# Kernel optimization log

Measured on AMD Instinct MI355X. Metric: run time of the kernel, lower is better.

Reference implementation:

```python
import jax, jax.numpy as jnp
import numpy as np

V, D, H, L, T, B = 32000, 512, 8, 4, 2048, 2
HS = D // H


def setup_inputs() -> dict:
    key = jax.random.key(0)
    ks = jax.random.split(key, 10)
    s = 0.02  # init std, per _init_weights
    rn = lambda k, shape: jax.random.normal(k, shape, jnp.float32) * s
    return {
        "idx": jax.random.randint(ks[0], (B, T), 0, V),
        "tok_emb": rn(ks[1], (V, D)),
        "pos_emb": rn(ks[2], (T, D)),
        "ln1_g": jnp.ones((L, D)), "ln1_b": jnp.zeros((L, D)),
        "wq": rn(ks[3], (L, D, D)), "wk": rn(ks[4], (L, D, D)), "wv": rn(ks[5], (L, D, D)),
        "wo": rn(ks[6], (L, D, D)), "bo": jnp.zeros((L, D)),
        "ln2_g": jnp.ones((L, D)), "ln2_b": jnp.zeros((L, D)),
        "w1": rn(ks[7], (L, D, 4 * D)), "b1": jnp.zeros((L, 4 * D)),
        "w2": rn(ks[8], (L, 4 * D, D)), "b2": jnp.zeros((L, D)),
        "lnf_g": jnp.ones((D,)), "lnf_b": jnp.zeros((D,)),
        "head_w": rn(ks[9], (D, V)), "head_b": jnp.zeros((V,)),
    }


def _ln(x, g, b):
    mu = x.mean(-1, keepdims=True)
    var = ((x - mu) ** 2).mean(-1, keepdims=True)
    return (x - mu) * jax.lax.rsqrt(var + 1e-5) * g + b


def reference(idx, tok_emb, pos_emb, ln1_g, ln1_b, wq, wk, wv, wo, bo,
              ln2_g, ln2_b, w1, b1, w2, b2, lnf_g, lnf_b, head_w, head_b):
    Bb, Tt = idx.shape
    x = tok_emb[idx] + pos_emb[jnp.arange(Tt)]  # [B,T,D]
    mask = jnp.tril(jnp.ones((Tt, Tt), bool))
    scale = HS ** -0.5

    def block(x, p):
        g1, bb1, Wq, Wk, Wv, Wo, Bo, g2, bb2, W1, B1, W2, B2 = p
        h = _ln(x, g1, bb1)
        q = (h @ Wq).reshape(Bb, Tt, H, HS)
        k = (h @ Wk).reshape(Bb, Tt, H, HS)
        v = (h @ Wv).reshape(Bb, Tt, H, HS)
        wei = jnp.einsum('bthd,bshd->bhts', q, k) * scale  # [B,H,T,T]
        wei = jnp.where(mask, wei, -jnp.inf)
        wei = jax.nn.softmax(wei, axis=-1)
        att = jnp.einsum('bhts,bshd->bthd', wei, v).reshape(Bb, Tt, D)
        x = x + att @ Wo + Bo
        h2 = _ln(x, g2, bb2)
        x = x + jax.nn.relu(h2 @ W1 + B1) @ W2 + B2
        return x, None

    x, _ = jax.lax.scan(block, x, (ln1_g, ln1_b, wq, wk, wv, wo, bo,
                                   ln2_g, ln2_b, w1, b1, w2, b2))
    logits = _ln(x, lnf_g, lnf_b) @ head_w + head_b  # [B,T,V]
    return logits
```

## Files before the change

### kernel.cpp

```cpp
#include <hip/hip_runtime.h>
#include <hip/hip_bf16.h>
#include <cstddef>

typedef __bf16 bf16;
typedef __attribute__((ext_vector_type(8))) __bf16 bf16x8;
typedef __attribute__((ext_vector_type(4))) __bf16 bf16x4;
typedef __attribute__((ext_vector_type(4))) float f32x4;

constexpr int VOC = 32000;
constexpr int DIM = 512;
constexpr int NH  = 8;
constexpr int HSZ = 64;
constexpr int SEQ = 2048;
constexpr int NB  = 2;
constexpr int NL  = 4;
constexpr int NTOK = NB * SEQ;
constexpr int QS  = 3 * DIM;
constexpr int QKS = 2 * DIM;

__device__ __forceinline__ void gload16(const void* g, void* lds) {
  __builtin_amdgcn_global_load_lds(
      (const __attribute__((address_space(1))) unsigned int*)g,
      (__attribute__((address_space(3))) unsigned int*)lds, 16, 0, 0);
}

__global__ __launch_bounds__(256) void wt_emln(
    const int* __restrict__ idx, const float* __restrict__ tok,
    const float* __restrict__ pos, const float* __restrict__ g1,
    const float* __restrict__ b1v, float* __restrict__ x, bf16* __restrict__ h,
    const float* __restrict__ wq, const float* __restrict__ wk,
    const float* __restrict__ wv, const float* __restrict__ wo,
    const float* __restrict__ w1, const float* __restrict__ w2,
    const float* __restrict__ hw,
    bf16* __restrict__ wqkvT, bf16* __restrict__ woT,
    bf16* __restrict__ w1T, bf16* __restrict__ w2T, bf16* __restrict__ headT) {
  __shared__ float t[32][33];
  __shared__ float s1[4], s2[4];
  int bid = blockIdx.x;
  int tid = threadIdx.x;
  if (bid < NTOK) {
    int row = bid;
    int lane = tid & 63, w = tid >> 6;
    int tt = row & (SEQ - 1);
    int tk = idx[row];
    float a0 = tok[(size_t)tk * DIM + tid] + pos[(size_t)tt * DIM + tid];
    float a1 = tok[(size_t)tk * DIM + tid + 256] + pos[(size_t)tt * DIM + tid + 256];
    x[(size_t)row * DIM + tid] = a0;
    x[(size_t)row * DIM + tid + 256] = a1;
    float ps = a0 + a1, pq = a0 * a0 + a1 * a1;
#pragma unroll
    for (int m = 1; m < 64; m <<= 1) {
      ps += __shfl_xor(ps, m, 64);
      pq += __shfl_xor(pq, m, 64);
    }
    if (lane == 0) { s1[w] = ps; s2[w] = pq; }
    __syncthreads();
    float fs = s1[0] + s1[1] + s1[2] + s1[3];
    float fq = s2[0] + s2[1] + s2[2] + s2[3];
    float mu = fs * (1.0f / DIM);
    float var = fq * (1.0f / DIM) - mu * mu;
    float rs = rsqrtf(var + 1e-5f);
    h[(size_t)row * DIM + tid] = (bf16)((a0 - mu) * rs * g1[tid] + b1v[tid]);
    h[(size_t)row * DIM + tid + 256] =
        (bf16)((a1 - mu) * rs * g1[tid + 256] + b1v[tid + 256]);
    return;
  }
  int wb = bid - NTOK;
  const float* src; bf16* dst; int K, N, n0, k0;
  if (wb < 12288) {
    int l = wb / 3072, tt = wb - l * 3072;
    if (tt < 1024) {
      int which = tt >> 8, u = tt & 255;
      K = DIM; N = DIM;
      n0 = (u & 15) * 32; k0 = (u >> 4) * 32;
      if (which == 0)      { src = wq + (size_t)l * DIM * DIM; dst = wqkvT + (size_t)l * QS * DIM; }
      else if (which == 1) { src = wk + (size_t)l * DIM * DIM; dst = wqkvT + (size_t)l * QS * DIM + DIM * DIM; }
      else if (which == 2) { src = wv + (size_t)l * DIM * DIM; dst = wqkvT + (size_t)l * QS * DIM + 2 * DIM * DIM; }
      else                 { src = wo + (size_t)l * DIM * DIM; dst = woT + (size_t)l * DIM * DIM; }
    } else if (tt < 2048) {
      int u = tt - 1024;
      K = DIM; N = 4 * DIM;
      n0 = (u & 63) * 32; k0 = (u >> 6) * 32;
      src = w1 + (size_t)l * DIM * 4 * DIM; dst = w1T + (size_t)l * 4 * DIM * DIM;
    } else {
      int u = tt - 2048;
      K = 4 * DIM; N = DIM;
      n0 = (u & 15) * 32; k0 = (u >> 4) * 32;
      src = w2 + (size_t)l * 4 * DIM * DIM; dst = w2T + (size_t)l * 4 * DIM * DIM;
    }
  } else {
    int u = wb - 12288;
    K = DIM; N = VOC;
    n0 = (u >> 4) * 32; k0 = (u & 15) * 32;
    src = hw; dst = headT;
  }
  int tx = tid & 31, ty = tid >> 5;
#pragma unroll
  for (int r = 0; r < 4; ++r)
    t[ty + r * 8][tx] = src[(size_t)(k0 + ty + r * 8) * N + n0 + tx];
  __syncthreads();
#pragma unroll
  for (int r = 0; r < 4; ++r)
    dst[(size_t)(n0 + ty + r * 8) * K + k0 + tx] = (bf16)t[tx][ty + r * 8];
}

__global__ __launch_bounds__(256) void ln_kernel(
    const float* __restrict__ x, const float* __restrict__ g,
    const float* __restrict__ b, bf16* __restrict__ out) {
  int row = blockIdx.x * 4 + (threadIdx.x >> 6);
  int lane = threadIdx.x & 63;
  const float* xr = x + (size_t)row * DIM + lane * 8;
  float4 v0 = *(const float4*)xr;
  float4 v1 = *(const float4*)(xr + 4);
  float ps = v0.x + v0.y + v0.z + v0.w + v1.x + v1.y + v1.z + v1.w;
  float pq = v0.x * v0.x + v0.y * v0.y + v0.z * v0.z + v0.w * v0.w +
             v1.x * v1.x + v1.y * v1.y + v1.z * v1.z + v1.w * v1.w;
#pragma unroll
  for (int m = 1; m < 64; m <<= 1) {
    ps += __shfl_xor(ps, m, 64);
    pq += __shfl_xor(pq, m, 64);
  }
  float mu = ps * (1.0f / DIM);
  float var = pq * (1.0f / DIM) - mu * mu;
  float rs = rsqrtf(var + 1e-5f);
  const float* gp = g + lane * 8;
  const float* bp = b + lane * 8;
  float4 g0 = *(const float4*)gp, g1v = *(const float4*)(gp + 4);
  float4 b0 = *(const float4*)bp, b1v = *(const float4*)(bp + 4);
  bf16x8 o;
  o[0] = (bf16)((v0.x - mu) * rs * g0.x + b0.x);
  o[1] = (bf16)((v0.y - mu) * rs * g0.y + b0.y);
  o[2] = (bf16)((v0.z - mu) * rs * g0.z + b0.z);
  o[3] = (bf16)((v0.w - mu) * rs * g0.w + b0.w);
  o[4] = (bf16)((v1.x - mu) * rs * g1v.x + b1v.x);
  o[5] = (bf16)((v1.y - mu) * rs * g1v.y + b1v.y);
  o[6] = (bf16)((v1.z - mu) * rs * g1v.z + b1v.z);
  o[7] = (bf16)((v1.w - mu) * rs * g1v.w + b1v.w);
  *(bf16x8*)(out + (size_t)row * DIM + lane * 8) = o;
}

template <int BM, int BN, bool RELU, bool RES, bool OUTB, bool VSPLIT>
__global__ __launch_bounds__((BM == 256) ? 512 : 256) void gemm_t(
    const bf16* __restrict__ A, const bf16* __restrict__ Wt,
    const float* __restrict__ bias, const float* __restrict__ res,
    float* __restrict__ outF, bf16* __restrict__ outB, bf16* __restrict__ vTout,
    int K, int N, int ostride) {
  constexpr int NW = (BM == 256) ? 8 : 4;
  constexpr int WN = (BN == 128) ? 2 : 1;
  constexpr int WM = NW / WN;
  constexpr int MP = BM / WM / 16;
  constexpr int NP = BN / WN / 16;
  constexpr int AJ = (BM * 128) / (NW * 1024);
  constexpr int BJ = (BN * 128) / (NW * 1024);
  __shared__ bf16 As[BM * 64];
  __shared__ bf16 Bs[BN * 64];
  int tid = threadIdx.x;
  int wid = tid >> 6, ln = tid & 63;
  int lr = ln & 15, lg = ln >> 4;
  int nmt = gridDim.x;
  int bid = blockIdx.y * nmt + blockIdx.x;
  int cpx = (gridDim.x * gridDim.y) >> 3;
  int swz = (bid & 7) * cpx + (bid >> 3);
  int m0 = (swz % nmt) * BM;
  int n0 = (swz / nmt) * BN;
  int wr = wid / WN, wc = wid % WN;
  f32x4 acc[MP][NP] = {};

  const char* Ab = (const char*)A;
  const char* Bb = (const char*)Wt;

  for (int k0 = 0; k0 < K; k0 += 64) {
    __syncthreads();
#pragma unroll
    for (int j = 0; j < AJ; ++j) {
      int Lb = j * (NW * 1024) + wid * 1024;
      int L = Lb + ln * 16;
      int row = L >> 7;
      int colb = (L & 127) ^ ((row & 7) << 4);
      gload16(Ab + (size_t)(m0 + row) * (K * 2) + (size_t)k0 * 2 + colb,
              (char*)As + Lb);
    }
#pragma unroll
    for (int j = 0; j < BJ; ++j) {
      int Lb = j * (NW * 1024) + wid * 1024;
      int L = Lb + ln * 16;
      int row = L >> 7;
      int colb = (L & 127) ^ ((row & 7) << 4);
      gload16(Bb + (size_t)(n0 + row) * (K * 2) + (size_t)k0 * 2 + colb,
              (char*)Bs + Lb);
    }
    __syncthreads();
#pragma unroll
    for (int kk = 0; kk < 2; ++kk) {
      bf16x8 am[MP], bn[NP];
#pragma unroll
      for (int m = 0; m < MP; ++m) {
        int row = wr * (BM / WM) + m * 16 + lr;
        int cb = (kk * 64 + lg * 16) ^ ((row & 7) << 4);
        am[m] = *(const bf16x8*)((const char*)As + row * 128 + cb);
      }
#pragma unroll
      for (int n = 0; n < NP; ++n) {
        int row = wc * (BN / WN) + n * 16 + lr;
        int cb = (kk * 64 + lg * 16) ^ ((row & 7) << 4);
        bn[n] = *(const bf16x8*)((const char*)Bs + row * 128 + cb);
      }
#pragma unroll
      for (int m = 0; m < MP; ++m)
#pragma unroll
        for (int n = 0; n < NP; ++n)
          acc[m][n] = __builtin_amdgcn_mfma_f32_16x16x32_bf16(
              am[m], bn[n], acc[m][n], 0, 0, 0);
    }
  }

  if (VSPLIT && n0 >= 2 * DIM) {
#pragma unroll
    for (int m = 0; m < MP; ++m) {
      int mrow = m0 + wr * (BM / WM) + m * 16 + lg * 4;
      int bb = mrow >> 11, tt = mrow & (SEQ - 1);
#pragma unroll
      for (int n = 0; n < NP; ++n) {
        int d = n0 + wc * (BN / WN) + n * 16 + lr - 2 * DIM;
        bf16x4 pk;
#pragma unroll
        for (int i = 0; i < 4; ++i) pk[i] = (bf16)acc[m][n][i];
        *(bf16x4*)(vTout + ((size_t)(bb * NH + (d >> 6)) * HSZ + (d & 63)) * SEQ + tt) = pk;
      }
    }
    return;
  }

  float qscale = (VSPLIT && n0 < DIM) ? 0.125f : 1.0f;
#pragma unroll
  for (int m = 0; m < MP; ++m) {
    int mrow = m0 + wr * (BM / WM) + m * 16 + lg * 4;
#pragma unroll
    for (int n = 0; n < NP; ++n) {
      int nc = n0 + wc * (BN / WN) + n * 16 + lr;
      float bval = bias ? bias[nc] : 0.0f;
#pragma unroll
      for (int i = 0; i < 4; ++i) {
        int mm = mrow + i;
        float val = acc[m][n][i] * qscale + bval;
        if (RELU) val = fmaxf(val, 0.0f);
        if (RES) val += res[(size_t)mm * ostride + nc];
        if (OUTB) outB[(size_t)mm * ostride + nc] = (bf16)val;
        else      outF[(size_t)mm * ostride + nc] = val;
      }
    }
  }
}

__global__ __launch_bounds__(256) void fattn_kernel(
    const bf16* __restrict__ qk, const bf16* __restrict__ vT,
    bf16* __restrict__ att) {
  __shared__ bf16 Ks[2][64 * 64];
  __shared__ bf16 Vs[2][64 * 64];
  __shared__ bf16 Pl[4][16][72];
  int tid = threadIdx.x;
  int wave = tid >> 6, lane = tid & 63;
  int lr = lane & 15, lg = lane >> 4;
  int h = blockIdx.y, b = blockIdx.z;
  int qt0 = ((b == 1) ? (gridDim.x - 1 - blockIdx.x) : blockIdx.x) * 64;
  const bf16* qb = qk + ((size_t)b * SEQ) * QKS + h * HSZ;
  const char* kb = (const char*)(qb + DIM);
  const char* vb = (const char*)(vT + (size_t)(b * NH + h) * HSZ * SEQ);

  bf16x8 aq[2];
  {
    const bf16* qr = qb + (size_t)(qt0 + wave * 16 + lr) * QKS + lg * 8;
    aq[0] = *(const bf16x8*)qr;
    aq[1] = *(const bf16x8*)(qr + 32);
  }

  f32x4 accO[4] = {};
  float l_r[4] = {0.f, 0.f, 0.f, 0.f};

  int ntile = qt0 / 64 + 1;
#define STAGE(ti, buf)                                                        \
  {                                                                           \
    _Pragma("unroll")                                                         \
    for (int j = 0; j < 2; ++j) {                                             \
      int Lb = j * 4096 + wave * 1024;                                        \
      int L = Lb + lane * 16;                                                 \
      int row = L >> 7;                                                       \
      int cb = (L & 127) ^ ((row & 7) << 4);                                  \
      gload16(kb + (size_t)((ti) * 64 + row) * (QKS * 2) + cb,                \
              (char*)Ks[buf] + Lb);                                           \
      gload16(vb + (size_t)row * (SEQ * 2) + (ti) * 128 + cb,                 \
              (char*)Vs[buf] + Lb);                                           \
    }                                                                         \
  }

  STAGE(0, 0);
  int cur = 0;
  for (int ti = 0; ti < ntile; ++ti) {
    if (ti + 1 < ntile) {
      STAGE(ti + 1, cur ^ 1);
      asm volatile("s_waitcnt vmcnt(4)" ::: "memory");
    } else {
      asm volatile("s_waitcnt vmcnt(0)" ::: "memory");
    }
    __builtin_amdgcn_s_barrier();
    int kv0 = ti * 64;
    bool diag = (ti == ntile - 1);

    f32x4 sc[4];
#pragma unroll
    for (int s = 0; s < 4; ++s) {
      int row = s * 16 + lr;
      const char* base = (const char*)Ks[cur] + row * 128;
      bf16x8 b0 = *(const bf16x8*)(base + ((lg * 16) ^ ((row & 7) << 4)));
      bf16x8 b1 = *(const bf16x8*)(base + ((64 + lg * 16) ^ ((row & 7) << 4)));
      f32x4 z = {};
      z = __builtin_amdgcn_mfma_f32_16x16x32_bf16(aq[0], b0, z, 0, 0, 0);
      sc[s] = __builtin_amdgcn_mfma_f32_16x16x32_bf16(aq[1], b1, z, 0, 0, 0);
    }

#pragma unroll
    for (int i = 0; i < 4; ++i) {
      if (diag) {
        int qrow = qt0 + wave * 16 + lg * 4 + i;
#pragma unroll
        for (int s = 0; s < 4; ++s) {
          int kvc = kv0 + s * 16 + lr;
          if (kvc > qrow) sc[s][i] = -1e30f;
        }
      }
      float rs = 0.f;
#pragma unroll
      for (int s = 0; s < 4; ++s) {
        float p = __expf(sc[s][i]);
        sc[s][i] = p;
        rs += p;
      }
      rs += __shfl_xor(rs, 1, 64);
      rs += __shfl_xor(rs, 2, 64);
      rs += __shfl_xor(rs, 4, 64);
      rs += __shfl_xor(rs, 8, 64);
      l_r[i] += rs;
    }

#pragma unroll
    for (int i = 0; i < 4; ++i)
#pragma unroll
      for (int s = 0; s < 4; ++s)
        Pl[wave][lg * 4 + i][s * 16 + lr] = (bf16)sc[s][i];
    bf16x8 pa0 = *(const bf16x8*)&Pl[wave][lr][lg * 8];
    bf16x8 pa1 = *(const bf16x8*)&Pl[wave][lr][32 + lg * 8];

#pragma unroll
    for (int ds = 0; ds < 4; ++ds) {
      int row = ds * 16 + lr;
      const char* base = (const char*)Vs[cur] + row * 128;
      bf16x8 v0 = *(const bf16x8*)(base + ((lg * 16) ^ ((row & 7) << 4)));
      bf16x8 v1 = *(const bf16x8*)(base + ((64 + lg * 16) ^ ((row & 7) << 4)));
      accO[ds] = __builtin_amdgcn_mfma_f32_16x16x32_bf16(pa0, v0, accO[ds], 0, 0, 0);
      accO[ds] = __builtin_amdgcn_mfma_f32_16x16x32_bf16(pa1, v1, accO[ds], 0, 0, 0);
    }
    __builtin_amdgcn_s_barrier();
    cur ^= 1;
  }
#undef STAGE

#pragma unroll
  for (int i = 0; i < 4; ++i) {
    float inv = 1.0f / l_r[i];
    size_t orow = ((size_t)b * SEQ + qt0 + wave * 16 + lg * 4 + i) * DIM + h * HSZ;
#pragma unroll
    for (int ds = 0; ds < 4; ++ds)
      att[orow + ds * 16 + lr] = (bf16)(accO[ds][i] * inv);
  }
}

extern "C" void kernel_launch(void* const* d_in, const int* in_sizes, int n_in,
                              void* d_out, int out_size, void* d_ws, size_t ws_size,
                              hipStream_t stream) {
  const int*   idx    = (const int*)d_in[0];
  const float* tok    = (const float*)d_in[1];
  const float* pos    = (const float*)d_in[2];
  const float* ln1_g  = (const float*)d_in[3];
  const float* ln1_b  = (const float*)d_in[4];
  const float* wq     = (const float*)d_in[5];
  const float* wk     = (const float*)d_in[6];
  const float* wv     = (const float*)d_in[7];
  const float* wo     = (const float*)d_in[8];
  const float* bo     = (const float*)d_in[9];
  const float* ln2_g  = (const float*)d_in[10];
  const float* ln2_b  = (const float*)d_in[11];
  const float* w1     = (const float*)d_in[12];
  const float* b1     = (const float*)d_in[13];
  const float* w2     = (const float*)d_in[14];
  const float* b2     = (const float*)d_in[15];
  const float* lnf_g  = (const float*)d_in[16];
  const float* lnf_b  = (const float*)d_in[17];
  const float* head_w = (const float*)d_in[18];
  const float* head_b = (const float*)d_in[19];

  char* W = (char*)d_ws;
  float* x     = (float*)(W);
  bf16*  h     = (bf16*)(W + 8388608);
  bf16*  qk    = (bf16*)(W + 12582912);
  bf16*  vTb   = (bf16*)(W + 20971520);
  bf16*  attb  = (bf16*)(W + 25165824);
  bf16*  ffn   = (bf16*)(W + 29360128);
  bf16*  wqkvT = (bf16*)(W + 46137344);
  bf16*  woT   = (bf16*)(W + 52428800);
  bf16*  w1T   = (bf16*)(W + 54525952);
  bf16*  w2T   = (bf16*)(W + 62914560);
  bf16*  headT = (bf16*)(W + 71303168);

  wt_emln<<<NTOK + 12288 + 16000, 256, 0, stream>>>(
      idx, tok, pos, ln1_g, ln1_b, x, h,
      wq, wk, wv, wo, w1, w2, head_w, wqkvT, woT, w1T, w2T, headT);

  dim3 gQKV(NTOK / 128, QS / 128);
  dim3 gD64(NTOK / 128, DIM / 64);
  dim3 gF1(NTOK / 128, 4 * DIM / 128);
  dim3 gV(NTOK / 128, VOC / 128);
  dim3 gA(SEQ / 64, NH, NB);

  for (int l = 0; l < NL; ++l) {
    if (l > 0)
      ln_kernel<<<NTOK / 4, 256, 0, stream>>>(x, ln1_g + l * DIM, ln1_b + l * DIM, h);
    gemm_t<128, 128, false, false, true, true><<<gQKV, 256, 0, stream>>>(
        h, wqkvT + (size_t)l * QS * DIM, nullptr, nullptr, nullptr, qk, vTb,
        DIM, QS, QKS);
    fattn_kernel<<<gA, 256, 0, stream>>>(qk, vTb, attb);
    gemm_t<128, 64, false, true, false, false><<<gD64, 256, 0, stream>>>(
        attb, woT + (size_t)l * DIM * DIM, bo + l * DIM, x, x, nullptr, nullptr,
        DIM, DIM, DIM);
    ln_kernel<<<NTOK / 4, 256, 0, stream>>>(x, ln2_g + l * DIM, ln2_b + l * DIM, h);
    gemm_t<128, 128, true, false, true, false><<<gF1, 256, 0, stream>>>(
        h, w1T + (size_t)l * 4 * DIM * DIM, b1 + (size_t)l * 4 * DIM, nullptr,
        nullptr, ffn, nullptr, DIM, 4 * DIM, 4 * DIM);
    gemm_t<128, 64, false, true, false, false><<<gD64, 256, 0, stream>>>(
        ffn, w2T + (size_t)l * 4 * DIM * DIM, b2 + l * DIM, x, x, nullptr,
        nullptr, 4 * DIM, DIM, DIM);
  }

  ln_kernel<<<NTOK / 4, 256, 0, stream>>>(x, lnf_g, lnf_b, h);
  gemm_t<128, 128, false, false, false, false><<<gV, 256, 0, stream>>>(
      h, headT, head_b, nullptr, (float*)d_out, nullptr, nullptr, DIM, VOC, VOC);
}
```

Measured before the change: 840.7 us.

## Double-buffer narrow GEMMs, widen head GEMM tile, enlarge transpose tiles, prioritize attention MFMAs

Adds an optional double-buffered LDS pipeline to the GEMM template, used for the two N=512 projection GEMMs, so the next K-slice loads while MFMAs run. The LM-head GEMM moves to a 128x256 tile with 512 threads to raise reuse of the A operand. Weight-transpose blocks grow from 32x32 to 64x64 tiles, so fewer blocks are launched. s_setprio is raised around the MFMA sections in flash attention. Risks: the hardcoded vmcnt count, larger LDS use lowering occupancy, and more registers in the wide head tile.

```diff
diff --git a/kernel.cpp b/kernel.cpp
--- a/kernel.cpp
+++ b/kernel.cpp
@@ -34,7 +34,7 @@
     const float* __restrict__ hw,
     bf16* __restrict__ wqkvT, bf16* __restrict__ woT,
     bf16* __restrict__ w1T, bf16* __restrict__ w2T, bf16* __restrict__ headT) {
-  __shared__ float t[32][33];
+  __shared__ float t[64][65];
   __shared__ float s1[4], s2[4];
   int bid = blockIdx.x;
   int tid = threadIdx.x;
@@ -67,41 +67,45 @@
   }
   int wb = bid - NTOK;
   const float* src; bf16* dst; int K, N, n0, k0;
-  if (wb < 12288) {
-    int l = wb / 3072, tt = wb - l * 3072;
-    if (tt < 1024) {
-      int which = tt >> 8, u = tt & 255;
+  if (wb < 3072) {
+    int l = wb / 768, tt = wb - l * 768;
+    if (tt < 256) {
+      int which = tt >> 6, u = tt & 63;
       K = DIM; N = DIM;
-      n0 = (u & 15) * 32; k0 = (u >> 4) * 32;
+      n0 = (u & 7) * 64; k0 = (u >> 3) * 64;
       if (which == 0)      { src = wq + (size_t)l * DIM * DIM; dst = wqkvT + (size_t)l * QS * DIM; }
       else if (which == 1) { src = wk + (size_t)l * DIM * DIM; dst = wqkvT + (size_t)l * QS * DIM + DIM * DIM; }
       else if (which == 2) { src = wv + (size_t)l * DIM * DIM; dst = wqkvT + (size_t)l * QS * DIM + 2 * DIM * DIM; }
       else                 { src = wo + (size_t)l * DIM * DIM; dst = woT + (size_t)l * DIM * DIM; }
-    } else if (tt < 2048) {
-      int u = tt - 1024;
+    } else if (tt < 512) {
+      int u = tt - 256;
       K = DIM; N = 4 * DIM;
-      n0 = (u & 63) * 32; k0 = (u >> 6) * 32;
+      n0 = (u & 31) * 64; k0 = (u >> 5) * 64;
       src = w1 + (size_t)l * DIM * 4 * DIM; dst = w1T + (size_t)l * 4 * DIM * DIM;
     } else {
-      int u = tt - 2048;
+      int u = tt - 512;
       K = 4 * DIM; N = DIM;
-      n0 = (u & 15) * 32; k0 = (u >> 4) * 32;
+      n0 = (u & 7) * 64; k0 = (u >> 3) * 64;
       src = w2 + (size_t)l * 4 * DIM * DIM; dst = w2T + (size_t)l * 4 * DIM * DIM;
     }
   } else {
-    int u = wb - 12288;
+    int u = wb - 3072;
     K = DIM; N = VOC;
-    n0 = (u >> 4) * 32; k0 = (u & 15) * 32;
+    n0 = (u >> 3) * 64; k0 = (u & 7) * 64;
     src = hw; dst = headT;
   }
-  int tx = tid & 31, ty = tid >> 5;
-#pragma unroll
-  for (int r = 0; r < 4; ++r)
-    t[ty + r * 8][tx] = src[(size_t)(k0 + ty + r * 8) * N + n0 + tx];
+  int tx = tid & 63, ty = tid >> 6;
+#pragma unroll
+  for (int r = 0; r < 16; ++r) {
+    int row = ty + r * 4;
+    t[row][tx] = src[(size_t)(k0 + row) * N + n0 + tx];
+  }
   __syncthreads();
 #pragma unroll
-  for (int r = 0; r < 4; ++r)
-    dst[(size_t)(n0 + ty + r * 8) * K + k0 + tx] = (bf16)t[tx][ty + r * 8];
+  for (int r = 0; r < 16; ++r) {
+    int row = ty + r * 4;
+    dst[(size_t)(n0 + row) * K + k0 + tx] = (bf16)t[tx][row];
+  }
 }
 
 __global__ __launch_bounds__(256) void ln_kernel(
@@ -139,21 +143,22 @@
   *(bf16x8*)(out + (size_t)row * DIM + lane * 8) = o;
 }
 
-template <int BM, int BN, bool RELU, bool RES, bool OUTB, bool VSPLIT>
-__global__ __launch_bounds__((BM == 256) ? 512 : 256) void gemm_t(
+template <int BM, int BN, bool RELU, bool RES, bool OUTB, bool VSPLIT, bool DB>
+__global__ __launch_bounds__((BN == 256) ? 512 : 256) void gemm_t(
     const bf16* __restrict__ A, const bf16* __restrict__ Wt,
     const float* __restrict__ bias, const float* __restrict__ res,
     float* __restrict__ outF, bf16* __restrict__ outB, bf16* __restrict__ vTout,
     int K, int N, int ostride) {
-  constexpr int NW = (BM == 256) ? 8 : 4;
-  constexpr int WN = (BN == 128) ? 2 : 1;
+  constexpr int NW = (BN == 256) ? 8 : 4;
+  constexpr int WN = (BN == 256) ? 4 : (BN == 128) ? 2 : 1;
   constexpr int WM = NW / WN;
   constexpr int MP = BM / WM / 16;
   constexpr int NP = BN / WN / 16;
   constexpr int AJ = (BM * 128) / (NW * 1024);
   constexpr int BJ = (BN * 128) / (NW * 1024);
-  __shared__ bf16 As[BM * 64];
-  __shared__ bf16 Bs[BN * 64];
+  static_assert(!DB || (AJ + BJ == 6), "DB vmcnt hardcoded for 6 loads");
+  __shared__ bf16 As[(DB ? 2 : 1) * BM * 64];
+  __shared__ bf16 Bs[(DB ? 2 : 1) * BN * 64];
   int tid = threadIdx.x;
   int wid = tid >> 6, ln = tid & 63;
   int lr = ln & 15, lg = ln >> 4;
@@ -169,16 +174,15 @@
   const char* Ab = (const char*)A;
   const char* Bb = (const char*)Wt;
 
-  for (int k0 = 0; k0 < K; k0 += 64) {
-    __syncthreads();
+  auto STAGE = [&](int k0s, int buf) {
 #pragma unroll
     for (int j = 0; j < AJ; ++j) {
       int Lb = j * (NW * 1024) + wid * 1024;
       int L = Lb + ln * 16;
       int row = L >> 7;
       int colb = (L & 127) ^ ((row & 7) << 4);
-      gload16(Ab + (size_t)(m0 + row) * (K * 2) + (size_t)k0 * 2 + colb,
-              (char*)As + Lb);
+      gload16(Ab + (size_t)(m0 + row) * (K * 2) + (size_t)k0s * 2 + colb,
+              (char*)As + buf * (BM * 128) + Lb);
     }
 #pragma unroll
     for (int j = 0; j < BJ; ++j) {
@@ -186,10 +190,27 @@
       int L = Lb + ln * 16;
       int row = L >> 7;
       int colb = (L & 127) ^ ((row & 7) << 4);
-      gload16(Bb + (size_t)(n0 + row) * (K * 2) + (size_t)k0 * 2 + colb,
-              (char*)Bs + Lb);
-    }
-    __syncthreads();
+      gload16(Bb + (size_t)(n0 + row) * (K * 2) + (size_t)k0s * 2 + colb,
+              (char*)Bs + buf * (BN * 128) + Lb);
+    }
+  };
+
+  if (DB) STAGE(0, 0);
+  int cur = 0;
+  for (int k0 = 0; k0 < K; k0 += 64) {
+    if (!DB) {
+      __syncthreads();
+      STAGE(k0, 0);
+      __syncthreads();
+    } else {
+      if (k0 + 64 < K) {
+        STAGE(k0 + 64, cur ^ 1);
+        asm volatile("s_waitcnt vmcnt(6)" ::: "memory");
+      } else {
+        asm volatile("s_waitcnt vmcnt(0)" ::: "memory");
+      }
+      __builtin_amdgcn_s_barrier();
+    }
 #pragma unroll
     for (int kk = 0; kk < 2; ++kk) {
       bf16x8 am[MP], bn[NP];
@@ -197,13 +218,13 @@
       for (int m = 0; m < MP; ++m) {
         int row = wr * (BM / WM) + m * 16 + lr;
         int cb = (kk * 64 + lg * 16) ^ ((row & 7) << 4);
-        am[m] = *(const bf16x8*)((const char*)As + row * 128 + cb);
+        am[m] = *(const bf16x8*)((const char*)As + cur * (BM * 128) + row * 128 + cb);
       }
 #pragma unroll
       for (int n = 0; n < NP; ++n) {
         int row = wc * (BN / WN) + n * 16 + lr;
         int cb = (kk * 64 + lg * 16) ^ ((row & 7) << 4);
-        bn[n] = *(const bf16x8*)((const char*)Bs + row * 128 + cb);
+        bn[n] = *(const bf16x8*)((const char*)Bs + cur * (BN * 128) + row * 128 + cb);
       }
 #pragma unroll
       for (int m = 0; m < MP; ++m)
@@ -211,6 +232,10 @@
         for (int n = 0; n < NP; ++n)
           acc[m][n] = __builtin_amdgcn_mfma_f32_16x16x32_bf16(
               am[m], bn[n], acc[m][n], 0, 0, 0);
+    }
+    if (DB) {
+      __builtin_amdgcn_s_barrier();
+      cur ^= 1;
     }
   }
 
@@ -307,6 +332,7 @@
     bool diag = (ti == ntile - 1);
 
     f32x4 sc[4];
+    __builtin_amdgcn_s_setprio(1);
 #pragma unroll
     for (int s = 0; s < 4; ++s) {
       int row = s * 16 + lr;
@@ -317,6 +343,7 @@
       z = __builtin_amdgcn_mfma_f32_16x16x32_bf16(aq[0], b0, z, 0, 0, 0);
       sc[s] = __builtin_amdgcn_mfma_f32_16x16x32_bf16(aq[1], b1, z, 0, 0, 0);
     }
+    __builtin_amdgcn_s_setprio(0);
 
 #pragma unroll
     for (int i = 0; i < 4; ++i) {
@@ -350,6 +377,7 @@
     bf16x8 pa0 = *(const bf16x8*)&Pl[wave][lr][lg * 8];
     bf16x8 pa1 = *(const bf16x8*)&Pl[wave][lr][32 + lg * 8];
 
+    __builtin_amdgcn_s_setprio(1);
 #pragma unroll
     for (int ds = 0; ds < 4; ++ds) {
       int row = ds * 16 + lr;
@@ -359,6 +387,7 @@
       accO[ds] = __builtin_amdgcn_mfma_f32_16x16x32_bf16(pa0, v0, accO[ds], 0, 0, 0);
       accO[ds] = __builtin_amdgcn_mfma_f32_16x16x32_bf16(pa1, v1, accO[ds], 0, 0, 0);
     }
+    __builtin_amdgcn_s_setprio(0);
     __builtin_amdgcn_s_barrier();
     cur ^= 1;
   }
@@ -411,36 +440,36 @@
   bf16*  w2T   = (bf16*)(W + 62914560);
   bf16*  headT = (bf16*)(W + 71303168);
 
-  wt_emln<<<NTOK + 12288 + 16000, 256, 0, stream>>>(
+  wt_emln<<<NTOK + 3072 + 4000, 256, 0, stream>>>(
       idx, tok, pos, ln1_g, ln1_b, x, h,
       wq, wk, wv, wo, w1, w2, head_w, wqkvT, woT, w1T, w2T, headT);
 
   dim3 gQKV(NTOK / 128, QS / 128);
   dim3 gD64(NTOK / 128, DIM / 64);
   dim3 gF1(NTOK / 128, 4 * DIM / 128);
-  dim3 gV(NTOK / 128, VOC / 128);
+  dim3 gV(NTOK / 128, VOC / 256);
   dim3 gA(SEQ / 64, NH, NB);
 
   for (int l = 0; l < NL; ++l) {
     if (l > 0)
       ln_kernel<<<NTOK / 4, 256, 0, stream>>>(x, ln1_g + l * DIM, ln1_b + l * DIM, h);
-    gemm_t<128, 128, false, false, true, true><<<gQKV, 256, 0, stream>>>(
+    gemm_t<128, 128, false, false, true, true, false><<<gQKV, 256, 0, stream>>>(
         h, wqkvT + (size_t)l * QS * DIM, nullptr, nullptr, nullptr, qk, vTb,
         DIM, QS, QKS);
     fattn_kernel<<<gA, 256, 0, stream>>>(qk, vTb, attb);
-    gemm_t<128, 64, false, true, false, false><<<gD64, 256, 0, stream>>>(
+    gemm_t<128, 64, false, true, false, false, true><<<gD64, 256, 0, stream>>>(
         attb, woT + (size_t)l * DIM * DIM, bo + l * DIM, x, x, nullptr, nullptr,
         DIM, DIM, DIM);
     ln_kernel<<<NTOK / 4, 256, 0, stream>>>(x, ln2_g + l * DIM, ln2_b + l * DIM, h);
-    gemm_t<128, 128, true, false, true, false><<<gF1, 256, 0, stream>>>(
+    gemm_t<128, 128, true, false, true, false, false><<<gF1, 256, 0, stream>>>(
         h, w1T + (size_t)l * 4 * DIM * DIM, b1 + (size_t)l * 4 * DIM, nullptr,
         nullptr, ffn, nullptr, DIM, 4 * DIM, 4 * DIM);
-    gemm_t<128, 64, false, true, false, false><<<gD64, 256, 0, stream>>>(
+    gemm_t<128, 64, false, true, false, false, true><<<gD64, 256, 0, stream>>>(
         ffn, w2T + (size_t)l * 4 * DIM * DIM, b2 + l * DIM, x, x, nullptr,
         nullptr, 4 * DIM, DIM, DIM);
   }
 
   ln_kernel<<<NTOK / 4, 256, 0, stream>>>(x, lnf_g, lnf_b, h);
-  gemm_t<128, 128, false, false, false, false><<<gV, 256, 0, stream>>>(
+  gemm_t<128, 256, false, false, false, false, false><<<gV, 512, 0, stream>>>(
       h, headT, head_b, nullptr, (float*)d_out, nullptr, nullptr, DIM, VOC, VOC);
 }
```

Result: faster. 804.9 us (-4.3%).
